# Performance work log

Hardware: AMD Instinct MI355X
Metric: run time of the kernel (lower is better)

The kernel has to match this reference:

```python
import jax, jax.numpy as jnp
import numpy as np

N_NODES = 100000
N_EDGES = 600000
IN_C, HID_C, OUT_C = 128, 128, 64


def setup_inputs() -> dict:
    key = jax.random.key(0)
    k1, k2, k3, k4 = jax.random.split(key, 4)
    x = jax.random.normal(k1, (N_NODES, IN_C), dtype=jnp.float32)
    edge_index = jax.random.randint(k2, (2, N_EDGES), 0, N_NODES, dtype=jnp.int64)
    # Glorot-ish init for linear weights
    W1 = jax.random.normal(k3, (IN_C, HID_C), dtype=jnp.float32) / np.sqrt(IN_C)
    b1 = jnp.zeros((HID_C,), dtype=jnp.float32)
    W2 = jax.random.normal(k4, (HID_C, OUT_C), dtype=jnp.float32) / np.sqrt(HID_C)
    b2 = jnp.zeros((OUT_C,), dtype=jnp.float32)
    prelu_a = jnp.full((1,), 0.25, dtype=jnp.float32)  # torch nn.PReLU default
    return {"x": x, "edge_index": edge_index, "W1": W1, "b1": b1,
            "W2": W2, "b2": b2, "prelu_a": prelu_a}


def _gcn_conv(x, src, dst, norm, W, b, num_nodes):
    # PyG GCNConv: h = x W; out[i] = sum_{(j->i)} norm_ji * h[j] + b
    h = x @ W                                   # [N, C_out]
    msg = h[src] * norm[:, None]                # [E', C_out] gather + scale
    out = jax.ops.segment_sum(msg, dst, num_segments=num_nodes)
    return out + b


def reference(x, edge_index, W1, b1, W2, b2, prelu_a):
    n = x.shape[0]
    # add self-loops
    loops = jnp.arange(n, dtype=edge_index.dtype)
    src = jnp.concatenate([edge_index[0], loops])
    dst = jnp.concatenate([edge_index[1], loops])
    # symmetric normalization deg^{-1/2}[src] * deg^{-1/2}[dst]
    deg = jax.ops.segment_sum(jnp.ones_like(dst, dtype=x.dtype), dst, num_segments=n)
    dinv = jnp.where(deg > 0, jax.lax.rsqrt(deg), 0.0)
    norm = dinv[src] * dinv[dst]
    # dropout p=0.0 -> identity
    h = _gcn_conv(x, src, dst, norm, W1, b1, n)
    h = jnp.where(h >= 0, h, prelu_a * h)       # PReLU (single shared parameter)
    out = _gcn_conv(h, src, dst, norm, W2, b2, n)
    return out
```

## Files before the change

### kernel.cpp

```cpp
#include <hip/hip_runtime.h>


typedef __attribute__((ext_vector_type(8))) short bf16x8;
typedef __attribute__((ext_vector_type(4))) float f32x4;

#define CAP 32
#define FB  64

__device__ inline unsigned short f2bf(float f) {
    unsigned int b = __float_as_uint(f);
    b += 0x7FFFu + ((b >> 16) & 1u);
    return (unsigned short)(b >> 16);
}
__device__ inline float bflo(unsigned int u) { return __uint_as_float(u << 16); }
__device__ inline float bfhi(unsigned int u) { return __uint_as_float(u & 0xFFFF0000u); }

__device__ inline void acc8(float* acc, uint4 v, float wgt) {
    acc[0] += bflo(v.x) * wgt; acc[1] += bfhi(v.x) * wgt;
    acc[2] += bflo(v.y) * wgt; acc[3] += bfhi(v.y) * wgt;
    acc[4] += bflo(v.z) * wgt; acc[5] += bfhi(v.z) * wgt;
    acc[6] += bflo(v.w) * wgt; acc[7] += bfhi(v.w) * wgt;
}

__global__ __launch_bounds__(512) void k_pre2(
    const float* __restrict__ W1, const float* __restrict__ W2,
    unsigned short* __restrict__ Wt1, unsigned short* __restrict__ Wt2,
    int* __restrict__ cnt, int n) {
    const int t = blockIdx.x * 512 + threadIdx.x;
    if (t < 128 * 128) {
        int nn = t >> 7, k = t & 127;
        Wt1[t] = f2bf(W1[k * 128 + nn]);
    } else if (t < 128 * 128 + 64 * 128) {
        int j = t - 128 * 128;
        int nn = j >> 7, k = j & 127;
        Wt2[j] = f2bf(W2[k * 64 + nn]);
    }
    const int n4 = n >> 2;
    for (int i = t; i < n4; i += gridDim.x * 512)
        ((int4*)cnt)[i] = make_int4(0, 0, 0, 0);
    if (blockIdx.x == 0 && threadIdx.x < (n & 3)) cnt[n4 * 4 + threadIdx.x] = 0;
}

__global__ __launch_bounds__(512) void k_conv1(
    const float* __restrict__ x, const unsigned short* __restrict__ Wt,
    unsigned short* __restrict__ H, int n,
    const int* __restrict__ esrc, const int* __restrict__ edst,
    int* __restrict__ cnt, int* __restrict__ bucket, int e) {
    constexpr int PITCH = 136;
    __shared__ unsigned short Bs[128 * PITCH];
    const int tid = threadIdx.x;

    if (blockIdx.x < FB) {
        const int t = blockIdx.x * 512 + tid;
        const int e4 = e >> 2;
        const int4* s4 = (const int4*)esrc;
        const int4* d4 = (const int4*)edst;
        for (int i = t; i < e4; i += FB * 512) {
            int4 s = s4[i], d = d4[i];
            int p0 = atomicAdd(&cnt[d.x], 1);
            int p1 = atomicAdd(&cnt[d.y], 1);
            int p2 = atomicAdd(&cnt[d.z], 1);
            int p3 = atomicAdd(&cnt[d.w], 1);
            if (p0 < CAP) bucket[(size_t)d.x * CAP + p0] = s.x;
            if (p1 < CAP) bucket[(size_t)d.y * CAP + p1] = s.y;
            if (p2 < CAP) bucket[(size_t)d.z * CAP + p2] = s.z;
            if (p3 < CAP) bucket[(size_t)d.w * CAP + p3] = s.w;
        }
        if (blockIdx.x == 0 && tid < (e & 3)) {
            int i = e4 * 4 + tid;
            int d = edst[i], s = esrc[i];
            int pos = atomicAdd(&cnt[d], 1);
            if (pos < CAP) bucket[(size_t)d * CAP + pos] = s;
        }
        return;
    }

    const int bx = blockIdx.x - FB;
    for (int q = tid; q < 128 * 16; q += 512) {
        int row = q >> 4, c16 = q & 15;
        *(uint4*)(Bs + row * PITCH + c16 * 8) =
            *(const uint4*)(Wt + row * 128 + c16 * 8);
    }

    const int wave = tid >> 6, lane = tid & 63;
    const int ml = lane & 15;
    const int g = lane >> 4;
    const int stripe = bx * 8 + wave;

    int ra = stripe * 16 + ml;
    if (ra >= n) ra = n - 1;

    bf16x8 af[4];
#pragma unroll
    for (int ks = 0; ks < 4; ++ks) {
        const float* p = x + (size_t)ra * 128 + ks * 32 + g * 8;
        float4 a0 = *(const float4*)p;
        float4 a1 = *(const float4*)(p + 4);
        uint4 pk;
        pk.x = (unsigned)f2bf(a0.x) | ((unsigned)f2bf(a0.y) << 16);
        pk.y = (unsigned)f2bf(a0.z) | ((unsigned)f2bf(a0.w) << 16);
        pk.z = (unsigned)f2bf(a1.x) | ((unsigned)f2bf(a1.y) << 16);
        pk.w = (unsigned)f2bf(a1.z) | ((unsigned)f2bf(a1.w) << 16);
        af[ks] = *(bf16x8*)&pk;
    }

    __syncthreads();

    f32x4 acc[8];
#pragma unroll
    for (int ct = 0; ct < 8; ++ct) acc[ct] = (f32x4){0.f, 0.f, 0.f, 0.f};

#pragma unroll
    for (int ks = 0; ks < 4; ++ks)
#pragma unroll
        for (int ct = 0; ct < 8; ++ct) {
            bf16x8 b = *(const bf16x8*)(Bs + (size_t)(ct * 16 + ml) * PITCH + ks * 32 + g * 8);
            acc[ct] = __builtin_amdgcn_mfma_f32_16x16x32_bf16(af[ks], b, acc[ct], 0, 0, 0);
        }

#pragma unroll
    for (int ct = 0; ct < 8; ++ct)
#pragma unroll
        for (int reg = 0; reg < 4; ++reg) {
            int r = stripe * 16 + g * 4 + reg;
            if (r < n) H[(size_t)r * 128 + ct * 16 + ml] = f2bf(acc[ct][reg]);
        }
}

__global__ __launch_bounds__(512) void k_gather_gemm(
    const unsigned short* __restrict__ H,
    const int* __restrict__ cnt, const int* __restrict__ bucket,
    const float* __restrict__ b1, const float* __restrict__ alpha_p,
    const unsigned short* __restrict__ Wt2,
    unsigned short* __restrict__ H2,
    int n) {
    constexpr int PITCH = 136;
    __shared__ unsigned short As[32 * PITCH];
    __shared__ unsigned short Bs[64 * PITCH];
    const int tid = threadIdx.x;

    for (int q = tid; q < 64 * 16; q += 512) {
        int row = q >> 4, c16 = q & 15;
        *(uint4*)(Bs + row * PITCH + c16 * 8) =
            *(const uint4*)(Wt2 + row * 128 + c16 * 8);
    }

    const int node = blockIdx.x * 32 + tid / 16;
    const int c0 = (tid & 15) * 8;
    const int lr = tid / 16;

    if (node < n) {
        int c = cnt[node];
        const float di = rsqrtf(1.0f + (float)c);
        if (c > CAP) c = CAP;

        float acc[8];
        {
            uint4 v = *(const uint4*)(H + (size_t)node * 128 + c0);
            float sl = di * di;
            acc[0] = bflo(v.x) * sl + b1[c0 + 0];
            acc[1] = bfhi(v.x) * sl + b1[c0 + 1];
            acc[2] = bflo(v.y) * sl + b1[c0 + 2];
            acc[3] = bfhi(v.y) * sl + b1[c0 + 3];
            acc[4] = bflo(v.z) * sl + b1[c0 + 4];
            acc[5] = bfhi(v.z) * sl + b1[c0 + 5];
            acc[6] = bflo(v.w) * sl + b1[c0 + 6];
            acc[7] = bfhi(v.w) * sl + b1[c0 + 7];
        }

        if (c > 0) {
            const int* bp = bucket + (size_t)node * CAP;
            int4 i0 = *(const int4*)bp;
            int4 i1 = *(const int4*)(bp + 4);
            int s0 = i0.x;
            int s1 = (1 < c) ? i0.y : s0;
            int s2 = (2 < c) ? i0.z : s0;
            int s3 = (3 < c) ? i0.w : s0;
            int s4 = (4 < c) ? i1.x : s0;
            int s5 = (5 < c) ? i1.y : s0;
            int s6 = (6 < c) ? i1.z : s0;
            int s7 = (7 < c) ? i1.w : s0;
            int cn0 = cnt[s0], cn1 = cnt[s1], cn2 = cnt[s2], cn3 = cnt[s3];
            int cn4 = cnt[s4], cn5 = cnt[s5], cn6 = cnt[s6], cn7 = cnt[s7];
            uint4 v0 = *(const uint4*)(H + (size_t)s0 * 128 + c0);
            uint4 v1 = *(const uint4*)(H + (size_t)s1 * 128 + c0);
            uint4 v2 = *(const uint4*)(H + (size_t)s2 * 128 + c0);
            uint4 v3 = *(const uint4*)(H + (size_t)s3 * 128 + c0);
            uint4 v4 = *(const uint4*)(H + (size_t)s4 * 128 + c0);
            uint4 v5 = *(const uint4*)(H + (size_t)s5 * 128 + c0);
            uint4 v6 = *(const uint4*)(H + (size_t)s6 * 128 + c0);
            uint4 v7 = *(const uint4*)(H + (size_t)s7 * 128 + c0);
            float w0 = rsqrtf(1.0f + (float)cn0) * di;
            float w1 = (1 < c) ? rsqrtf(1.0f + (float)cn1) * di : 0.0f;
            float w2 = (2 < c) ? rsqrtf(1.0f + (float)cn2) * di : 0.0f;
            float w3 = (3 < c) ? rsqrtf(1.0f + (float)cn3) * di : 0.0f;
            float w4 = (4 < c) ? rsqrtf(1.0f + (float)cn4) * di : 0.0f;
            float w5 = (5 < c) ? rsqrtf(1.0f + (float)cn5) * di : 0.0f;
            float w6 = (6 < c) ? rsqrtf(1.0f + (float)cn6) * di : 0.0f;
            float w7 = (7 < c) ? rsqrtf(1.0f + (float)cn7) * di : 0.0f;
            acc8(acc, v0, w0); acc8(acc, v1, w1);
            acc8(acc, v2, w2); acc8(acc, v3, w3);
            acc8(acc, v4, w4); acc8(acc, v5, w5);
            acc8(acc, v6, w6); acc8(acc, v7, w7);

            for (int q = 2; q * 4 < c; ++q) {
                int4 idx = *(const int4*)(bp + q * 4);
                int base = q * 4;
                int t0 = idx.x;
                int t1 = (base + 1 < c) ? idx.y : t0;
                int t2 = (base + 2 < c) ? idx.z : t0;
                int t3 = (base + 3 < c) ? idx.w : t0;
                int d0 = cnt[t0], d1 = cnt[t1], d2 = cnt[t2], d3 = cnt[t3];
                uint4 u0 = *(const uint4*)(H + (size_t)t0 * 128 + c0);
                uint4 u1 = *(const uint4*)(H + (size_t)t1 * 128 + c0);
                uint4 u2 = *(const uint4*)(H + (size_t)t2 * 128 + c0);
                uint4 u3 = *(const uint4*)(H + (size_t)t3 * 128 + c0);
                float y0 = rsqrtf(1.0f + (float)d0) * di;
                float y1 = (base + 1 < c) ? rsqrtf(1.0f + (float)d1) * di : 0.0f;
                float y2 = (base + 2 < c) ? rsqrtf(1.0f + (float)d2) * di : 0.0f;
                float y3 = (base + 3 < c) ? rsqrtf(1.0f + (float)d3) * di : 0.0f;
                acc8(acc, u0, y0); acc8(acc, u1, y1);
                acc8(acc, u2, y2); acc8(acc, u3, y3);
            }
        }

        float al = alpha_p[0];
        unsigned short o[8];
#pragma unroll
        for (int j = 0; j < 8; ++j) {
            float t = acc[j];
            t = (t >= 0.f) ? t : al * t;
            o[j] = f2bf(t);
        }
        uint4 pk;
        pk.x = (unsigned)o[0] | ((unsigned)o[1] << 16);
        pk.y = (unsigned)o[2] | ((unsigned)o[3] << 16);
        pk.z = (unsigned)o[4] | ((unsigned)o[5] << 16);
        pk.w = (unsigned)o[6] | ((unsigned)o[7] << 16);
        *(uint4*)(As + lr * PITCH + c0) = pk;
    }
    __syncthreads();

    const int wave = tid >> 6, lane = tid & 63;
    const int ml = lane & 15, g = lane >> 4;
    const int stripe = wave >> 2;
    const int ct = wave & 3;

    bf16x8 af[4];
#pragma unroll
    for (int ks = 0; ks < 4; ++ks)
        af[ks] = *(const bf16x8*)(As + (size_t)(stripe * 16 + ml) * PITCH + ks * 32 + g * 8);

    f32x4 acc2 = (f32x4){0.f, 0.f, 0.f, 0.f};
#pragma unroll
    for (int ks = 0; ks < 4; ++ks) {
        bf16x8 bb = *(const bf16x8*)(Bs + (size_t)(ct * 16 + ml) * PITCH + ks * 32 + g * 8);
        acc2 = __builtin_amdgcn_mfma_f32_16x16x32_bf16(af[ks], bb, acc2, 0, 0, 0);
    }

#pragma unroll
    for (int reg = 0; reg < 4; ++reg) {
        int r = blockIdx.x * 32 + stripe * 16 + g * 4 + reg;
        if (r < n) H2[(size_t)r * 64 + ct * 16 + ml] = f2bf(acc2[reg]);
    }
}

__global__ void k_gather2(const unsigned short* __restrict__ H,
                          const int* __restrict__ cnt, const int* __restrict__ bucket,
                          const float* __restrict__ b, float* __restrict__ out,
                          int n) {
    constexpr int COLS = 64;
    constexpr int NT = COLS / 8;
    constexpr int G = 256 / NT;
    const int tid = threadIdx.x;
    const int node = blockIdx.x * G + tid / NT;
    if (node >= n) return;
    const int c0 = (tid & (NT - 1)) * 8;

    int c = cnt[node];
    const float di = rsqrtf(1.0f + (float)c);
    if (c > CAP) c = CAP;

    float acc[8];
    {
        uint4 v = *(const uint4*)(H + (size_t)node * COLS + c0);
        float sl = di * di;
        acc[0] = bflo(v.x) * sl + b[c0 + 0];
        acc[1] = bfhi(v.x) * sl + b[c0 + 1];
        acc[2] = bflo(v.y) * sl + b[c0 + 2];
        acc[3] = bfhi(v.y) * sl + b[c0 + 3];
        acc[4] = bflo(v.z) * sl + b[c0 + 4];
        acc[5] = bfhi(v.z) * sl + b[c0 + 5];
        acc[6] = bflo(v.w) * sl + b[c0 + 6];
        acc[7] = bfhi(v.w) * sl + b[c0 + 7];
    }

    if (c > 0) {
        const int* bp = bucket + (size_t)node * CAP;
        int4 i0 = *(const int4*)bp;
        int4 i1 = *(const int4*)(bp + 4);
        int s0 = i0.x;
        int s1 = (1 < c) ? i0.y : s0;
        int s2 = (2 < c) ? i0.z : s0;
        int s3 = (3 < c) ? i0.w : s0;
        int s4 = (4 < c) ? i1.x : s0;
        int s5 = (5 < c) ? i1.y : s0;
        int s6 = (6 < c) ? i1.z : s0;
        int s7 = (7 < c) ? i1.w : s0;
        int cn0 = cnt[s0], cn1 = cnt[s1], cn2 = cnt[s2], cn3 = cnt[s3];
        int cn4 = cnt[s4], cn5 = cnt[s5], cn6 = cnt[s6], cn7 = cnt[s7];
        uint4 v0 = *(const uint4*)(H + (size_t)s0 * COLS + c0);
        uint4 v1 = *(const uint4*)(H + (size_t)s1 * COLS + c0);
        uint4 v2 = *(const uint4*)(H + (size_t)s2 * COLS + c0);
        uint4 v3 = *(const uint4*)(H + (size_t)s3 * COLS + c0);
        uint4 v4 = *(const uint4*)(H + (size_t)s4 * COLS + c0);
        uint4 v5 = *(const uint4*)(H + (size_t)s5 * COLS + c0);
        uint4 v6 = *(const uint4*)(H + (size_t)s6 * COLS + c0);
        uint4 v7 = *(const uint4*)(H + (size_t)s7 * COLS + c0);
        float w0 = rsqrtf(1.0f + (float)cn0) * di;
        float w1 = (1 < c) ? rsqrtf(1.0f + (float)cn1) * di : 0.0f;
        float w2 = (2 < c) ? rsqrtf(1.0f + (float)cn2) * di : 0.0f;
        float w3 = (3 < c) ? rsqrtf(1.0f + (float)cn3) * di : 0.0f;
        float w4 = (4 < c) ? rsqrtf(1.0f + (float)cn4) * di : 0.0f;
        float w5 = (5 < c) ? rsqrtf(1.0f + (float)cn5) * di : 0.0f;
        float w6 = (6 < c) ? rsqrtf(1.0f + (float)cn6) * di : 0.0f;
        float w7 = (7 < c) ? rsqrtf(1.0f + (float)cn7) * di : 0.0f;
        acc8(acc, v0, w0); acc8(acc, v1, w1);
        acc8(acc, v2, w2); acc8(acc, v3, w3);
        acc8(acc, v4, w4); acc8(acc, v5, w5);
        acc8(acc, v6, w6); acc8(acc, v7, w7);

        for (int q = 2; q * 4 < c; ++q) {
            int4 idx = *(const int4*)(bp + q * 4);
            int base = q * 4;
            int t0 = idx.x;
            int t1 = (base + 1 < c) ? idx.y : t0;
            int t2 = (base + 2 < c) ? idx.z : t0;
            int t3 = (base + 3 < c) ? idx.w : t0;
            int d0 = cnt[t0], d1 = cnt[t1], d2 = cnt[t2], d3 = cnt[t3];
            uint4 u0 = *(const uint4*)(H + (size_t)t0 * COLS + c0);
            uint4 u1 = *(const uint4*)(H + (size_t)t1 * COLS + c0);
            uint4 u2 = *(const uint4*)(H + (size_t)t2 * COLS + c0);
            uint4 u3 = *(const uint4*)(H + (size_t)t3 * COLS + c0);
            float y0 = rsqrtf(1.0f + (float)d0) * di;
            float y1 = (base + 1 < c) ? rsqrtf(1.0f + (float)d1) * di : 0.0f;
            float y2 = (base + 2 < c) ? rsqrtf(1.0f + (float)d2) * di : 0.0f;
            float y3 = (base + 3 < c) ? rsqrtf(1.0f + (float)d3) * di : 0.0f;
            acc8(acc, u0, y0); acc8(acc, u1, y1);
            acc8(acc, u2, y2); acc8(acc, u3, y3);
        }
    }

    *(float4*)(out + (size_t)node * COLS + c0) =
        make_float4(acc[0], acc[1], acc[2], acc[3]);
    *(float4*)(out + (size_t)node * COLS + c0 + 4) =
        make_float4(acc[4], acc[5], acc[6], acc[7]);
}

extern "C" void kernel_launch(void* const* d_in, const int* in_sizes, int n_in,
                              void* d_out, int out_size, void* d_ws, size_t ws_size,
                              hipStream_t stream) {
    const float* x  = (const float*)d_in[0];
    const int*   ei = (const int*)d_in[1];
    const float* W1 = (const float*)d_in[2];
    const float* b1 = (const float*)d_in[3];
    const float* W2 = (const float*)d_in[4];
    const float* b2 = (const float*)d_in[5];
    const float* pa = (const float*)d_in[6];
    float* out = (float*)d_out;

    const int n = in_sizes[0] / 128;
    const int e = in_sizes[1] / 2;
    const int* src = ei;
    const int* dst = ei + e;

    unsigned short* h1  = (unsigned short*)d_ws;
    unsigned short* h2  = h1 + (size_t)n * 128;
    unsigned short* Wt1 = h2 + (size_t)n * 64;
    unsigned short* Wt2 = Wt1 + 128 * 128;
    int* cnt     = (int*)(Wt2 + 64 * 128);
    int* bucket  = cnt + n;

    const int gblk = ((n + 15) / 16 + 7) / 8;

    k_pre2<<<64, 512, 0, stream>>>(W1, W2, Wt1, Wt2, cnt, n);
    k_conv1<<<FB + gblk, 512, 0, stream>>>(x, Wt1, h1, n, src, dst,
                                           cnt, bucket, e);
    k_gather_gemm<<<(n + 31) / 32, 512, 0, stream>>>(h1, cnt, bucket, b1, pa,
                                                     Wt2, h2, n);
    k_gather2<<<(n + 31) / 32, 256, 0, stream>>>(h2, cnt, bucket, b2, out, n);
}
```

Before: 201.3 us.

## Pre-scale features by dinv to drop per-edge degree lookups in gathers

Factors the symmetric normalization so each source row is pre-multiplied by its dinv. The gathers then only sum rows and apply the destination dinv once, which removes the per-neighbor cnt lookups and rsqrt calls. This needs a new k_scale pass that reads an fp32 H1 written by conv1 and writes a scaled bf16 copy, adding about 100k x 128 x (4+4+2) bytes of extra memory traffic. Fill blocks are also interleaved among the GEMM blocks (every fourth block) instead of occupying the leading block ids, and source indices are now clamped to the valid range.

```diff
diff --git a/kernel.cpp b/kernel.cpp
--- a/kernel.cpp
+++ b/kernel.cpp
@@ -5,7 +5,6 @@
 typedef __attribute__((ext_vector_type(4))) float f32x4;
 
 #define CAP 32
-#define FB  64
 
 __device__ inline unsigned short f2bf(float f) {
     unsigned int b = __float_as_uint(f);
@@ -15,11 +14,15 @@
 __device__ inline float bflo(unsigned int u) { return __uint_as_float(u << 16); }
 __device__ inline float bfhi(unsigned int u) { return __uint_as_float(u & 0xFFFF0000u); }
 
-__device__ inline void acc8(float* acc, uint4 v, float wgt) {
-    acc[0] += bflo(v.x) * wgt; acc[1] += bfhi(v.x) * wgt;
-    acc[2] += bflo(v.y) * wgt; acc[3] += bfhi(v.y) * wgt;
-    acc[4] += bflo(v.z) * wgt; acc[5] += bfhi(v.z) * wgt;
-    acc[6] += bflo(v.w) * wgt; acc[7] += bfhi(v.w) * wgt;
+__device__ inline int clampi(int s, int n) {
+    return ((unsigned)s < (unsigned)n) ? s : 0;
+}
+
+__device__ inline void acc8m(float* acc, uint4 v, float m) {
+    acc[0] += bflo(v.x) * m; acc[1] += bfhi(v.x) * m;
+    acc[2] += bflo(v.y) * m; acc[3] += bfhi(v.y) * m;
+    acc[4] += bflo(v.z) * m; acc[5] += bfhi(v.z) * m;
+    acc[6] += bflo(v.w) * m; acc[7] += bfhi(v.w) * m;
 }
 
 __global__ __launch_bounds__(512) void k_pre2(
@@ -43,19 +46,21 @@
 
 __global__ __launch_bounds__(512) void k_conv1(
     const float* __restrict__ x, const unsigned short* __restrict__ Wt,
-    unsigned short* __restrict__ H, int n,
+    float* __restrict__ H1f, int n,
     const int* __restrict__ esrc, const int* __restrict__ edst,
-    int* __restrict__ cnt, int* __restrict__ bucket, int e) {
+    int* __restrict__ cnt, int* __restrict__ bucket, int e, int nfill) {
     constexpr int PITCH = 136;
     __shared__ unsigned short Bs[128 * PITCH];
     const int tid = threadIdx.x;
-
-    if (blockIdx.x < FB) {
-        const int t = blockIdx.x * 512 + tid;
+    const int b = blockIdx.x;
+
+    if ((b & 3) == 3) {
+        const int fid = b >> 2;
+        const int t = fid * 512 + tid;
         const int e4 = e >> 2;
         const int4* s4 = (const int4*)esrc;
         const int4* d4 = (const int4*)edst;
-        for (int i = t; i < e4; i += FB * 512) {
+        for (int i = t; i < e4; i += nfill * 512) {
             int4 s = s4[i], d = d4[i];
             int p0 = atomicAdd(&cnt[d.x], 1);
             int p1 = atomicAdd(&cnt[d.y], 1);
@@ -66,7 +71,7 @@
             if (p2 < CAP) bucket[(size_t)d.z * CAP + p2] = s.z;
             if (p3 < CAP) bucket[(size_t)d.w * CAP + p3] = s.w;
         }
-        if (blockIdx.x == 0 && tid < (e & 3)) {
+        if (fid == 0 && tid < (e & 3)) {
             int i = e4 * 4 + tid;
             int d = edst[i], s = esrc[i];
             int pos = atomicAdd(&cnt[d], 1);
@@ -75,7 +80,7 @@
         return;
     }
 
-    const int bx = blockIdx.x - FB;
+    const int bx = b - (b >> 2);
     for (int q = tid; q < 128 * 16; q += 512) {
         int row = q >> 4, c16 = q & 15;
         *(uint4*)(Bs + row * PITCH + c16 * 8) =
@@ -114,8 +119,8 @@
     for (int ks = 0; ks < 4; ++ks)
 #pragma unroll
         for (int ct = 0; ct < 8; ++ct) {
-            bf16x8 b = *(const bf16x8*)(Bs + (size_t)(ct * 16 + ml) * PITCH + ks * 32 + g * 8);
-            acc[ct] = __builtin_amdgcn_mfma_f32_16x16x32_bf16(af[ks], b, acc[ct], 0, 0, 0);
+            bf16x8 bb = *(const bf16x8*)(Bs + (size_t)(ct * 16 + ml) * PITCH + ks * 32 + g * 8);
+            acc[ct] = __builtin_amdgcn_mfma_f32_16x16x32_bf16(af[ks], bb, acc[ct], 0, 0, 0);
         }
 
 #pragma unroll
@@ -123,16 +128,37 @@
 #pragma unroll
         for (int reg = 0; reg < 4; ++reg) {
             int r = stripe * 16 + g * 4 + reg;
-            if (r < n) H[(size_t)r * 128 + ct * 16 + ml] = f2bf(acc[ct][reg]);
-        }
+            if (r < n) H1f[(size_t)r * 128 + ct * 16 + ml] = acc[ct][reg];
+        }
+}
+
+__global__ __launch_bounds__(256) void k_scale(
+    const float* __restrict__ H1f, const int* __restrict__ cnt,
+    unsigned short* __restrict__ h1s, float* __restrict__ dinv, int n) {
+    const int tid = threadIdx.x;
+    const int node = blockIdx.x * 16 + tid / 16;
+    if (node >= n) return;
+    const int c0 = (tid & 15) * 8;
+    const float di = rsqrtf(1.0f + (float)cnt[node]);
+    if ((tid & 15) == 0) dinv[node] = di;
+    const float* p = H1f + (size_t)node * 128 + c0;
+    float4 a0 = *(const float4*)p;
+    float4 a1 = *(const float4*)(p + 4);
+    uint4 pk;
+    pk.x = (unsigned)f2bf(a0.x * di) | ((unsigned)f2bf(a0.y * di) << 16);
+    pk.y = (unsigned)f2bf(a0.z * di) | ((unsigned)f2bf(a0.w * di) << 16);
+    pk.z = (unsigned)f2bf(a1.x * di) | ((unsigned)f2bf(a1.y * di) << 16);
+    pk.w = (unsigned)f2bf(a1.z * di) | ((unsigned)f2bf(a1.w * di) << 16);
+    *(uint4*)(h1s + (size_t)node * 128 + c0) = pk;
 }
 
 __global__ __launch_bounds__(512) void k_gather_gemm(
-    const unsigned short* __restrict__ H,
-    const int* __restrict__ cnt, const int* __restrict__ bucket,
+    const unsigned short* __restrict__ Hs,
+    const int* __restrict__ cnt, const float* __restrict__ dinv,
+    const int* __restrict__ bucket,
     const float* __restrict__ b1, const float* __restrict__ alpha_p,
     const unsigned short* __restrict__ Wt2,
-    unsigned short* __restrict__ H2,
+    unsigned short* __restrict__ H2s,
     int n) {
     constexpr int PITCH = 136;
     __shared__ unsigned short As[32 * PITCH];
@@ -151,84 +177,70 @@
 
     if (node < n) {
         int c = cnt[node];
-        const float di = rsqrtf(1.0f + (float)c);
+        const float di = dinv[node];
         if (c > CAP) c = CAP;
 
         float acc[8];
         {
-            uint4 v = *(const uint4*)(H + (size_t)node * 128 + c0);
-            float sl = di * di;
-            acc[0] = bflo(v.x) * sl + b1[c0 + 0];
-            acc[1] = bfhi(v.x) * sl + b1[c0 + 1];
-            acc[2] = bflo(v.y) * sl + b1[c0 + 2];
-            acc[3] = bfhi(v.y) * sl + b1[c0 + 3];
-            acc[4] = bflo(v.z) * sl + b1[c0 + 4];
-            acc[5] = bfhi(v.z) * sl + b1[c0 + 5];
-            acc[6] = bflo(v.w) * sl + b1[c0 + 6];
-            acc[7] = bfhi(v.w) * sl + b1[c0 + 7];
+            uint4 v = *(const uint4*)(Hs + (size_t)node * 128 + c0);
+            acc[0] = bflo(v.x); acc[1] = bfhi(v.x);
+            acc[2] = bflo(v.y); acc[3] = bfhi(v.y);
+            acc[4] = bflo(v.z); acc[5] = bfhi(v.z);
+            acc[6] = bflo(v.w); acc[7] = bfhi(v.w);
         }
 
         if (c > 0) {
             const int* bp = bucket + (size_t)node * CAP;
             int4 i0 = *(const int4*)bp;
             int4 i1 = *(const int4*)(bp + 4);
-            int s0 = i0.x;
-            int s1 = (1 < c) ? i0.y : s0;
-            int s2 = (2 < c) ? i0.z : s0;
-            int s3 = (3 < c) ? i0.w : s0;
-            int s4 = (4 < c) ? i1.x : s0;
-            int s5 = (5 < c) ? i1.y : s0;
-            int s6 = (6 < c) ? i1.z : s0;
-            int s7 = (7 < c) ? i1.w : s0;
-            int cn0 = cnt[s0], cn1 = cnt[s1], cn2 = cnt[s2], cn3 = cnt[s3];
-            int cn4 = cnt[s4], cn5 = cnt[s5], cn6 = cnt[s6], cn7 = cnt[s7];
-            uint4 v0 = *(const uint4*)(H + (size_t)s0 * 128 + c0);
-            uint4 v1 = *(const uint4*)(H + (size_t)s1 * 128 + c0);
-            uint4 v2 = *(const uint4*)(H + (size_t)s2 * 128 + c0);
-            uint4 v3 = *(const uint4*)(H + (size_t)s3 * 128 + c0);
-            uint4 v4 = *(const uint4*)(H + (size_t)s4 * 128 + c0);
-            uint4 v5 = *(const uint4*)(H + (size_t)s5 * 128 + c0);
-            uint4 v6 = *(const uint4*)(H + (size_t)s6 * 128 + c0);
-            uint4 v7 = *(const uint4*)(H + (size_t)s7 * 128 + c0);
-            float w0 = rsqrtf(1.0f + (float)cn0) * di;
-            float w1 = (1 < c) ? rsqrtf(1.0f + (float)cn1) * di : 0.0f;
-            float w2 = (2 < c) ? rsqrtf(1.0f + (float)cn2) * di : 0.0f;
-            float w3 = (3 < c) ? rsqrtf(1.0f + (float)cn3) * di : 0.0f;
-            float w4 = (4 < c) ? rsqrtf(1.0f + (float)cn4) * di : 0.0f;
-            float w5 = (5 < c) ? rsqrtf(1.0f + (float)cn5) * di : 0.0f;
-            float w6 = (6 < c) ? rsqrtf(1.0f + (float)cn6) * di : 0.0f;
-            float w7 = (7 < c) ? rsqrtf(1.0f + (float)cn7) * di : 0.0f;
-            acc8(acc, v0, w0); acc8(acc, v1, w1);
-            acc8(acc, v2, w2); acc8(acc, v3, w3);
-            acc8(acc, v4, w4); acc8(acc, v5, w5);
-            acc8(acc, v6, w6); acc8(acc, v7, w7);
+            int s0 = clampi(i0.x, n);
+            int s1 = (1 < c) ? clampi(i0.y, n) : s0;
+            int s2 = (2 < c) ? clampi(i0.z, n) : s0;
+            int s3 = (3 < c) ? clampi(i0.w, n) : s0;
+            int s4 = (4 < c) ? clampi(i1.x, n) : s0;
+            int s5 = (5 < c) ? clampi(i1.y, n) : s0;
+            int s6 = (6 < c) ? clampi(i1.z, n) : s0;
+            int s7 = (7 < c) ? clampi(i1.w, n) : s0;
+            uint4 v0 = *(const uint4*)(Hs + (size_t)s0 * 128 + c0);
+            uint4 v1 = *(const uint4*)(Hs + (size_t)s1 * 128 + c0);
+            uint4 v2 = *(const uint4*)(Hs + (size_t)s2 * 128 + c0);
+            uint4 v3 = *(const uint4*)(Hs + (size_t)s3 * 128 + c0);
+            uint4 v4 = *(const uint4*)(Hs + (size_t)s4 * 128 + c0);
+            uint4 v5 = *(const uint4*)(Hs + (size_t)s5 * 128 + c0);
+            uint4 v6 = *(const uint4*)(Hs + (size_t)s6 * 128 + c0);
+            uint4 v7 = *(const uint4*)(Hs + (size_t)s7 * 128 + c0);
+            acc8m(acc, v0, 1.0f);
+            acc8m(acc, v1, (1 < c) ? 1.0f : 0.0f);
+            acc8m(acc, v2, (2 < c) ? 1.0f : 0.0f);
+            acc8m(acc, v3, (3 < c) ? 1.0f : 0.0f);
+            acc8m(acc, v4, (4 < c) ? 1.0f : 0.0f);
+            acc8m(acc, v5, (5 < c) ? 1.0f : 0.0f);
+            acc8m(acc, v6, (6 < c) ? 1.0f : 0.0f);
+            acc8m(acc, v7, (7 < c) ? 1.0f : 0.0f);
 
             for (int q = 2; q * 4 < c; ++q) {
                 int4 idx = *(const int4*)(bp + q * 4);
                 int base = q * 4;
-                int t0 = idx.x;
-                int t1 = (base + 1 < c) ? idx.y : t0;
-                int t2 = (base + 2 < c) ? idx.z : t0;
-                int t3 = (base + 3 < c) ? idx.w : t0;
-                int d0 = cnt[t0], d1 = cnt[t1], d2 = cnt[t2], d3 = cnt[t3];
-                uint4 u0 = *(const uint4*)(H + (size_t)t0 * 128 + c0);
-                uint4 u1 = *(const uint4*)(H + (size_t)t1 * 128 + c0);
-                uint4 u2 = *(const uint4*)(H + (size_t)t2 * 128 + c0);
-                uint4 u3 = *(const uint4*)(H + (size_t)t3 * 128 + c0);
-                float y0 = rsqrtf(1.0f + (float)d0) * di;
-                float y1 = (base + 1 < c) ? rsqrtf(1.0f + (float)d1) * di : 0.0f;
-                float y2 = (base + 2 < c) ? rsqrtf(1.0f + (float)d2) * di : 0.0f;
-                float y3 = (base + 3 < c) ? rsqrtf(1.0f + (float)d3) * di : 0.0f;
-                acc8(acc, u0, y0); acc8(acc, u1, y1);
-                acc8(acc, u2, y2); acc8(acc, u3, y3);
+                int t0 = clampi(idx.x, n);
+                int t1 = (base + 1 < c) ? clampi(idx.y, n) : t0;
+                int t2 = (base + 2 < c) ? clampi(idx.z, n) : t0;
+                int t3 = (base + 3 < c) ? clampi(idx.w, n) : t0;
+                uint4 u0 = *(const uint4*)(Hs + (size_t)t0 * 128 + c0);
+                uint4 u1 = *(const uint4*)(Hs + (size_t)t1 * 128 + c0);
+                uint4 u2 = *(const uint4*)(Hs + (size_t)t2 * 128 + c0);
+                uint4 u3 = *(const uint4*)(Hs + (size_t)t3 * 128 + c0);
+                acc8m(acc, u0, 1.0f);
+                acc8m(acc, u1, (base + 1 < c) ? 1.0f : 0.0f);
+                acc8m(acc, u2, (base + 2 < c) ? 1.0f : 0.0f);
+                acc8m(acc, u3, (base + 3 < c) ? 1.0f : 0.0f);
             }
         }
 
-        float al = alpha_p[0];
+        const float al = alpha_p[0];
         unsigned short o[8];
 #pragma unroll
         for (int j = 0; j < 8; ++j) {
-            float t = acc[j];
+            float t = acc[j] * di + b1[c0 + j];
             t = (t >= 0.f) ? t : al * t;
             o[j] = f2bf(t);
         }
@@ -261,12 +273,14 @@
 #pragma unroll
     for (int reg = 0; reg < 4; ++reg) {
         int r = blockIdx.x * 32 + stripe * 16 + g * 4 + reg;
-        if (r < n) H2[(size_t)r * 64 + ct * 16 + ml] = f2bf(acc2[reg]);
-    }
-}
-
-__global__ void k_gather2(const unsigned short* __restrict__ H,
-                          const int* __restrict__ cnt, const int* __restrict__ bucket,
+        if (r < n)
+            H2s[(size_t)r * 64 + ct * 16 + ml] = f2bf(acc2[reg] * dinv[r]);
+    }
+}
+
+__global__ void k_gather2(const unsigned short* __restrict__ Hs,
+                          const int* __restrict__ cnt, const float* __restrict__ dinv,
+                          const int* __restrict__ bucket,
                           const float* __restrict__ b, float* __restrict__ out,
                           int n) {
     constexpr int COLS = 64;
@@ -278,83 +292,71 @@
     const int c0 = (tid & (NT - 1)) * 8;
 
     int c = cnt[node];
-    const float di = rsqrtf(1.0f + (float)c);
+    const float di = dinv[node];
     if (c > CAP) c = CAP;
 
     float acc[8];
     {
-        uint4 v = *(const uint4*)(H + (size_t)node * COLS + c0);
-        float sl = di * di;
-        acc[0] = bflo(v.x) * sl + b[c0 + 0];
-        acc[1] = bfhi(v.x) * sl + b[c0 + 1];
-        acc[2] = bflo(v.y) * sl + b[c0 + 2];
-        acc[3] = bfhi(v.y) * sl + b[c0 + 3];
-        acc[4] = bflo(v.z) * sl + b[c0 + 4];
-        acc[5] = bfhi(v.z) * sl + b[c0 + 5];
-        acc[6] = bflo(v.w) * sl + b[c0 + 6];
-        acc[7] = bfhi(v.w) * sl + b[c0 + 7];
+        uint4 v = *(const uint4*)(Hs + (size_t)node * COLS + c0);
+        acc[0] = bflo(v.x); acc[1] = bfhi(v.x);
+        acc[2] = bflo(v.y); acc[3] = bfhi(v.y);
+        acc[4] = bflo(v.z); acc[5] = bfhi(v.z);
+        acc[6] = bflo(v.w); acc[7] = bfhi(v.w);
     }
 
     if (c > 0) {
         const int* bp = bucket + (size_t)node * CAP;
         int4 i0 = *(const int4*)bp;
         int4 i1 = *(const int4*)(bp + 4);
-        int s0 = i0.x;
-        int s1 = (1 < c) ? i0.y : s0;
-        int s2 = (2 < c) ? i0.z : s0;
-        int s3 = (3 < c) ? i0.w : s0;
-        int s4 = (4 < c) ? i1.x : s0;
-        int s5 = (5 < c) ? i1.y : s0;
-        int s6 = (6 < c) ? i1.z : s0;
-        int s7 = (7 < c) ? i1.w : s0;
-        int cn0 = cnt[s0], cn1 = cnt[s1], cn2 = cnt[s2], cn3 = cnt[s3];
-        int cn4 = cnt[s4], cn5 = cnt[s5], cn6 = cnt[s6], cn7 = cnt[s7];
-        uint4 v0 = *(const uint4*)(H + (size_t)s0 * COLS + c0);
-        uint4 v1 = *(const uint4*)(H + (size_t)s1 * COLS + c0);
-        uint4 v2 = *(const uint4*)(H + (size_t)s2 * COLS + c0);
-        uint4 v3 = *(const uint4*)(H + (size_t)s3 * COLS + c0);
-        uint4 v4 = *(const uint4*)(H + (size_t)s4 * COLS + c0);
-        uint4 v5 = *(const uint4*)(H + (size_t)s5 * COLS + c0);
-        uint4 v6 = *(const uint4*)(H + (size_t)s6 * COLS + c0);
-        uint4 v7 = *(const uint4*)(H + (size_t)s7 * COLS + c0);
-        float w0 = rsqrtf(1.0f + (float)cn0) * di;
-        float w1 = (1 < c) ? rsqrtf(1.0f + (float)cn1) * di : 0.0f;
-        float w2 = (2 < c) ? rsqrtf(1.0f + (float)cn2) * di : 0.0f;
-        float w3 = (3 < c) ? rsqrtf(1.0f + (float)cn3) * di : 0.0f;
-        float w4 = (4 < c) ? rsqrtf(1.0f + (float)cn4) * di : 0.0f;
-        float w5 = (5 < c) ? rsqrtf(1.0f + (float)cn5) * di : 0.0f;
-        float w6 = (6 < c) ? rsqrtf(1.0f + (float)cn6) * di : 0.0f;
-        float w7 = (7 < c) ? rsqrtf(1.0f + (float)cn7) * di : 0.0f;
-        acc8(acc, v0, w0); acc8(acc, v1, w1);
-        acc8(acc, v2, w2); acc8(acc, v3, w3);
-        acc8(acc, v4, w4); acc8(acc, v5, w5);
-        acc8(acc, v6, w6); acc8(acc, v7, w7);
+        int s0 = clampi(i0.x, n);
+        int s1 = (1 < c) ? clampi(i0.y, n) : s0;
+        int s2 = (2 < c) ? clampi(i0.z, n) : s0;
+        int s3 = (3 < c) ? clampi(i0.w, n) : s0;
+        int s4 = (4 < c) ? clampi(i1.x, n) : s0;
+        int s5 = (5 < c) ? clampi(i1.y, n) : s0;
+        int s6 = (6 < c) ? clampi(i1.z, n) : s0;
+        int s7 = (7 < c) ? clampi(i1.w, n) : s0;
+        uint4 v0 = *(const uint4*)(Hs + (size_t)s0 * COLS + c0);
+        uint4 v1 = *(const uint4*)(Hs + (size_t)s1 * COLS + c0);
+        uint4 v2 = *(const uint4*)(Hs + (size_t)s2 * COLS + c0);
+        uint4 v3 = *(const uint4*)(Hs + (size_t)s3 * COLS + c0);
+        uint4 v4 = *(const uint4*)(Hs + (size_t)s4 * COLS + c0);
+        uint4 v5 = *(const uint4*)(Hs + (size_t)s5 * COLS + c0);
+        uint4 v6 = *(const uint4*)(Hs + (size_t)s6 * COLS + c0);
+        uint4 v7 = *(const uint4*)(Hs + (size_t)s7 * COLS + c0);
+        acc8m(acc, v0, 1.0f);
+        acc8m(acc, v1, (1 < c) ? 1.0f : 0.0f);
+        acc8m(acc, v2, (2 < c) ? 1.0f : 0.0f);
+        acc8m(acc, v3, (3 < c) ? 1.0f : 0.0f);
+        acc8m(acc, v4, (4 < c) ? 1.0f : 0.0f);
+        acc8m(acc, v5, (5 < c) ? 1.0f : 0.0f);
+        acc8m(acc, v6, (6 < c) ? 1.0f : 0.0f);
+        acc8m(acc, v7, (7 < c) ? 1.0f : 0.0f);
 
         for (int q = 2; q * 4 < c; ++q) {
             int4 idx = *(const int4*)(bp + q * 4);
             int base = q * 4;
-            int t0 = idx.x;
-            int t1 = (base + 1 < c) ? idx.y : t0;
-            int t2 = (base + 2 < c) ? idx.z : t0;
-            int t3 = (base + 3 < c) ? idx.w : t0;
-            int d0 = cnt[t0], d1 = cnt[t1], d2 = cnt[t2], d3 = cnt[t3];
-            uint4 u0 = *(const uint4*)(H + (size_t)t0 * COLS + c0);
-            uint4 u1 = *(const uint4*)(H + (size_t)t1 * COLS + c0);
-            uint4 u2 = *(const uint4*)(H + (size_t)t2 * COLS + c0);
-            uint4 u3 = *(const uint4*)(H + (size_t)t3 * COLS + c0);
-            float y0 = rsqrtf(1.0f + (float)d0) * di;
-            float y1 = (base + 1 < c) ? rsqrtf(1.0f + (float)d1) * di : 0.0f;
-            float y2 = (base + 2 < c) ? rsqrtf(1.0f + (float)d2) * di : 0.0f;
-            float y3 = (base + 3 < c) ? rsqrtf(1.0f + (float)d3) * di : 0.0f;
-            acc8(acc, u0, y0); acc8(acc, u1, y1);
-            acc8(acc, u2, y2); acc8(acc, u3, y3);
+            int t0 = clampi(idx.x, n);
+            int t1 = (base + 1 < c) ? clampi(idx.y, n) : t0;
+            int t2 = (base + 2 < c) ? clampi(idx.z, n) : t0;
+            int t3 = (base + 3 < c) ? clampi(idx.w, n) : t0;
+            uint4 u0 = *(const uint4*)(Hs + (size_t)t0 * COLS + c0);
+            uint4 u1 = *(const uint4*)(Hs + (size_t)t1 * COLS + c0);
+            uint4 u2 = *(const uint4*)(Hs + (size_t)t2 * COLS + c0);
+            uint4 u3 = *(const uint4*)(Hs + (size_t)t3 * COLS + c0);
+            acc8m(acc, u0, 1.0f);
+            acc8m(acc, u1, (base + 1 < c) ? 1.0f : 0.0f);
+            acc8m(acc, u2, (base + 2 < c) ? 1.0f : 0.0f);
+            acc8m(acc, u3, (base + 3 < c) ? 1.0f : 0.0f);
         }
     }
 
     *(float4*)(out + (size_t)node * COLS + c0) =
-        make_float4(acc[0], acc[1], acc[2], acc[3]);
+        make_float4(acc[0] * di + b[c0 + 0], acc[1] * di + b[c0 + 1],
+                    acc[2] * di + b[c0 + 2], acc[3] * di + b[c0 + 3]);
     *(float4*)(out + (size_t)node * COLS + c0 + 4) =
-        make_float4(acc[4], acc[5], acc[6], acc[7]);
+        make_float4(acc[4] * di + b[c0 + 4], acc[5] * di + b[c0 + 5],
+                    acc[6] * di + b[c0 + 6], acc[7] * di + b[c0 + 7]);
 }
 
 extern "C" void kernel_launch(void* const* d_in, const int* in_sizes, int n_in,
@@ -374,19 +376,25 @@
     const int* src = ei;
     const int* dst = ei + e;
 
-    unsigned short* h1  = (unsigned short*)d_ws;
-    unsigned short* h2  = h1 + (size_t)n * 128;
-    unsigned short* Wt1 = h2 + (size_t)n * 64;
+    float*          H1f = (float*)d_ws;
+    unsigned short* h1s = (unsigned short*)(H1f + (size_t)n * 128);
+    unsigned short* h2s = h1s + (size_t)n * 128;
+    unsigned short* Wt1 = h2s + (size_t)n * 64;
     unsigned short* Wt2 = Wt1 + 128 * 128;
-    int* cnt     = (int*)(Wt2 + 64 * 128);
-    int* bucket  = cnt + n;
+    float* dinv  = (float*)(Wt2 + 64 * 128);
+    int*   cnt   = (int*)(dinv + n);
+    int*   bucket = cnt + n;
 
     const int gblk = ((n + 15) / 16 + 7) / 8;
+    const int T = (gblk * 4 + 2) / 3;
+    const int nfill = T >> 2;
 
     k_pre2<<<64, 512, 0, stream>>>(W1, W2, Wt1, Wt2, cnt, n);
-    k_conv1<<<FB + gblk, 512, 0, stream>>>(x, Wt1, h1, n, src, dst,
-                                           cnt, bucket, e);
-    k_gather_gemm<<<(n + 31) / 32, 512, 0, stream>>>(h1, cnt, bucket, b1, pa,
-                                                     Wt2, h2, n);
-    k_gather2<<<(n + 31) / 32, 256, 0, stream>>>(h2, cnt, bucket, b2, out, n);
-}
+    k_conv1<<<T, 512, 0, stream>>>(x, Wt1, H1f, n, src, dst, cnt, bucket,
+                                   e, nfill);
+    k_scale<<<(n + 15) / 16, 256, 0, stream>>>(H1f, cnt, h1s, dinv, n);
+    k_gather_gemm<<<(n + 31) / 32, 512, 0, stream>>>(h1s, cnt, dinv, bucket,
+                                                     b1, pa, Wt2, h2s, n);
+    k_gather2<<<(n + 31) / 32, 256, 0, stream>>>(h2s, cnt, dinv, bucket,
+                                                 b2, out, n);
+}
```

Measured after the change: 214.7 us. 1.07x slower.
